# Performance work log

Measured on AMD Instinct MI355X. Metric: run time of the kernel, lower is better.

## Reference

```python
import jax, jax.numpy as jnp
import numpy as np

N_BASIS = 20
R_MAX = 3.5

# e3nn normalize2mom constant for silu: 1/sqrt(E[silu(z)^2]), z~N(0,1) (analytic quadrature)
_trapz = getattr(np, "trapezoid", np.trapz)
_z = np.linspace(-12.0, 12.0, 100001)
_phi = np.exp(-0.5 * _z**2) / np.sqrt(2.0 * np.pi)
_silu = _z / (1.0 + np.exp(-_z))
SILU_CST = float(1.0 / np.sqrt(_trapz(_silu**2 * _phi, _z)))  # ~1.679


def norm_silu(x):
    return SILU_CST * jax.nn.silu(x)


def spherical_harmonics_lmax3(pos):
    # component-normalized real spherical harmonics up to l=3, e3nn axis convention (y up)
    u = pos / jnp.linalg.norm(pos, axis=-1, keepdims=True)
    x, y, z = u[..., 0], u[..., 1], u[..., 2]
    x2, y2, z2 = x * x, y * y, z * z
    s3, s5, s15 = jnp.sqrt(3.0), jnp.sqrt(5.0), jnp.sqrt(15.0)
    s7, s105 = jnp.sqrt(7.0), jnp.sqrt(105.0)
    s35_8, s21_8 = jnp.sqrt(35.0 / 8.0), jnp.sqrt(21.0 / 8.0)
    sh = [
        jnp.ones_like(x),                                                   # l=0
        s3 * x, s3 * y, s3 * z,                                             # l=1
        s15 * x * z, s15 * x * y, s5 * (y2 - 0.5 * (x2 + z2)),
        s15 * y * z, 0.5 * s15 * (z2 - x2),                                 # l=2
        s35_8 * x * (3.0 * z2 - x2), s105 * x * y * z,
        s21_8 * x * (5.0 * y2 - 1.0), 0.5 * s7 * y * (5.0 * y2 - 3.0),
        s21_8 * z * (5.0 * y2 - 1.0), 0.5 * s105 * y * (z2 - x2),
        s35_8 * z * (z2 - 3.0 * x2),                                        # l=3
    ]
    return jnp.stack(sh, axis=-1)  # [E, 16]


def soft_one_hot_gaussian(d):
    # e3nn soft_one_hot_linspace(start=0, end=3.5, number=20, basis='gaussian', cutoff=True)
    values = jnp.linspace(0.0, R_MAX, N_BASIS + 2)[1:-1]
    step = R_MAX / (N_BASIS + 1)
    diff = (d[:, None] - values[None, :]) / step
    return jnp.exp(-diff * diff) / 1.12


def setup_inputs() -> dict:
    E, N = 2_000_000, 125_000
    key = jax.random.key(0)
    k = jax.random.split(key, 6)
    return {
        "pos": jax.random.normal(k[0], (E, 3), jnp.float32),
        "x_right": jax.random.normal(k[1], (E, 1), jnp.float32),
        "x_left": jax.random.normal(k[2], (N, 1), jnp.float32),
        "W1": jax.random.normal(k[3], (20, 30), jnp.float32),
        "W2": jax.random.normal(k[4], (30, 5), jnp.float32),
        "origin_index": jax.random.randint(k[5], (E,), 0, N),
    }


def reference(pos, x_right, x_left, W1, W2, origin_index):
    sh = spherical_harmonics_lmax3(pos)                 # [E, 16], component norm
    d = jnp.linalg.norm(pos, axis=-1)                   # [E]
    emb = soft_one_hot_gaussian(d)                      # [E, 20]
    # e3nn FullyConnectedNet([20, 30, 5], silu): x @ W / sqrt(fan_in), normalized act on hidden
    h = norm_silu(emb @ (W1 / jnp.sqrt(jnp.asarray(W1.shape[0], jnp.float32))))
    tp_weights = h @ (W2 / jnp.sqrt(jnp.asarray(W2.shape[0], jnp.float32)))  # [E, 5]
    # tp1: FullyConnectedTensorProduct('1x0e', sh, '5x0e'): only CG path is 0e(x)0e->0e
    # (single path -> path-normalization factor 1; Y_0 = 1 under component normalization)
    h_right = tp_weights * x_right * sh[:, :1]          # [E, 5]
    # tp2: FullTensorProduct('1x0e', '5x0e') -> '5x0e': plain scalar product per channel
    product = x_left[origin_index] * h_right            # [E, 5]
    return jnp.sum(product)
```

## Files before the change

kernel.cpp:

```cpp
#include <hip/hip_runtime.h>


#define TN    2048
#define DMAXF 5.0f
#define TPB   256
#define EPT   8
#define TILE  (TPB * EPT)

__device__ __constant__ float kSiluCst = 1.6765581f;

__global__ __launch_bounds__(256) void build_lut_kernel(
    const float* __restrict__ W1, const float* __restrict__ W2,
    float* __restrict__ table, float* __restrict__ out)
{
    if (blockIdx.x == 0 && threadIdx.x == 0) out[0] = 0.0f;

    int t = blockIdx.x * 256 + threadIdx.x;
    int entry = t >> 5;
    int k = t & 31;
    int kk = (k < 30) ? k : 29;

    float d  = (float)entry * (DMAXF / (float)TN);
    float t6 = 6.0f * d;
    const float w1scale = 1.0f / (1.12f * sqrtf(20.0f));

    float a = 0.0f;
    #pragma unroll
    for (int j = 0; j < 20; ++j) {
        float df = t6 - (float)(j + 1);
        float e  = __expf(-df * df);
        a = fmaf(e * w1scale, W1[j * 30 + kk], a);
    }
    float s = a / (1.0f + __expf(-a));

    float w2s = 0.0f;
    #pragma unroll
    for (int c = 0; c < 5; ++c) w2s += W2[kk * 5 + c];

    float contrib = (k < 30) ? s * w2s * (kSiluCst / sqrtf(30.0f)) : 0.0f;

    #pragma unroll
    for (int m = 16; m > 0; m >>= 1) contrib += __shfl_xor(contrib, m, 32);

    if (k == 0 && entry < TN) table[entry] = contrib;
}

__global__ __launch_bounds__(TPB) void edge_sum_kernel(
    const float* __restrict__ pos, const float* __restrict__ xr,
    const float* __restrict__ xl, const int* __restrict__ oi,
    const float* __restrict__ table, float* __restrict__ out, int E)
{
    __shared__ float lut[TN];
    __shared__ double swv[TPB / 64];

    const int tid = threadIdx.x;

    {
        const float4* t4 = (const float4*)table;
        float4* l4 = (float4*)lut;
        l4[tid]       = t4[tid];
        l4[tid + TPB] = t4[tid + TPB];
    }
    __syncthreads();

    const float scale = (float)TN / DMAXF;
    const float umax  = (float)(TN - 1) - 1e-3f;

    const long tile0 = (long)blockIdx.x * TILE;
    const int  rem   = (int)min((long)TILE, (long)E - tile0);
    const int  e0    = tid * EPT;
    double acc = 0.0;

    if (e0 + EPT <= rem) {
        const long g0 = tile0 + e0;
        const float4* p4 = (const float4*)(pos + g0 * 3);
        float4 P0 = p4[0], P1 = p4[1], P2 = p4[2], P3 = p4[3], P4 = p4[4], P5 = p4[5];
        const float4* x4 = (const float4*)(xr + g0);
        float4 X0 = x4[0], X1 = x4[1];
        const int4* o4 = (const int4*)(oi + g0);
        int4 O0 = o4[0], O1 = o4[1];

        float xlv[EPT];
        xlv[0] = xl[O0.x]; xlv[1] = xl[O0.y]; xlv[2] = xl[O0.z]; xlv[3] = xl[O0.w];
        xlv[4] = xl[O1.x]; xlv[5] = xl[O1.y]; xlv[6] = xl[O1.z]; xlv[7] = xl[O1.w];

        float px[EPT] = {P0.x, P0.w, P1.z, P2.y, P3.x, P3.w, P4.z, P5.y};
        float py[EPT] = {P0.y, P1.x, P1.w, P2.z, P3.y, P4.x, P4.w, P5.z};
        float pz[EPT] = {P0.z, P1.y, P2.x, P2.w, P3.z, P4.y, P5.x, P5.w};
        float xrv[EPT] = {X0.x, X0.y, X0.z, X0.w, X1.x, X1.y, X1.z, X1.w};

        float fsum = 0.0f;
        #pragma unroll
        for (int j = 0; j < EPT; ++j) {
            float d  = sqrtf(fmaf(px[j], px[j], fmaf(py[j], py[j], pz[j] * pz[j])));
            float u  = fminf(d * scale, umax);
            int   i0 = (int)u;
            float fr = u - (float)i0;
            float f  = fmaf(fr, lut[i0 + 1] - lut[i0], lut[i0]);
            fsum = fmaf(f * xrv[j], xlv[j], fsum);
        }
        acc = (double)fsum;
    } else if (e0 < rem) {
        float fsum = 0.0f;
        for (int j = 0; j < EPT && e0 + j < rem; ++j) {
            long  ge = tile0 + e0 + j;
            float x = pos[3 * ge], y = pos[3 * ge + 1], z = pos[3 * ge + 2];
            float d  = sqrtf(fmaf(x, x, fmaf(y, y, z * z)));
            float u  = fminf(d * scale, umax);
            int   i0 = (int)u;
            float fr = u - (float)i0;
            float f  = fmaf(fr, lut[i0 + 1] - lut[i0], lut[i0]);
            fsum = fmaf(f * xr[ge], xl[oi[ge]], fsum);
        }
        acc = (double)fsum;
    }

    #pragma unroll
    for (int off = 32; off > 0; off >>= 1) acc += __shfl_down(acc, off);
    int lane = tid & 63, wv = tid >> 6;
    if (lane == 0) swv[wv] = acc;
    __syncthreads();
    if (tid == 0) {
        double bsum = (swv[0] + swv[1]) + (swv[2] + swv[3]);
        atomicAdd(out, (float)bsum);
    }
}

extern "C" void kernel_launch(void* const* d_in, const int* in_sizes, int n_in,
                              void* d_out, int out_size, void* d_ws, size_t ws_size,
                              hipStream_t stream) {
    const float* pos = (const float*)d_in[0];
    const float* xr  = (const float*)d_in[1];
    const float* xl  = (const float*)d_in[2];
    const float* W1  = (const float*)d_in[3];
    const float* W2  = (const float*)d_in[4];
    const int*   oi  = (const int*)d_in[5];
    float* out = (float*)d_out;

    int E = in_sizes[1];
    int nblk = (E + TILE - 1) / TILE;

    float* table = (float*)d_ws;

    hipLaunchKernelGGL(build_lut_kernel, dim3((TN * 32) / 256), dim3(256), 0, stream,
                       W1, W2, table, out);
    hipLaunchKernelGGL(edge_sum_kernel, dim3(nblk), dim3(TPB), 0, stream,
                       pos, xr, xl, oi, table, out, E);
}
```

Before: 28.03 us.

## Split edge reduction into a per-edge value kernel and a gather-reduce kernel

Splits the fused edge kernel in two. The first kernel computes the LUT-interpolated radial factor times x_right and writes it to a workspace buffer. The second kernel gathers x_left by origin_index, multiplies, and does the reduction. The likely intent is to separate the gather latency from the LUT and sqrt work so each kernel has simpler register and memory behaviour. The cost is an extra 8 MB write and read of the intermediate per call, plus one more kernel launch.

Measured after the change: 36.50 us. +30.2%, slower.

```diff
diff --git a/kernel.cpp b/kernel.cpp
--- a/kernel.cpp
+++ b/kernel.cpp
@@ -45,14 +45,11 @@
     if (k == 0 && entry < TN) table[entry] = contrib;
 }
 
-__global__ __launch_bounds__(TPB) void edge_sum_kernel(
+__global__ __launch_bounds__(TPB) void val_kernel(
     const float* __restrict__ pos, const float* __restrict__ xr,
-    const float* __restrict__ xl, const int* __restrict__ oi,
-    const float* __restrict__ table, float* __restrict__ out, int E)
+    const float* __restrict__ table, float* __restrict__ val, int E)
 {
     __shared__ float lut[TN];
-    __shared__ double swv[TPB / 64];
-
     const int tid = threadIdx.x;
 
     {
@@ -69,27 +66,20 @@
     const long tile0 = (long)blockIdx.x * TILE;
     const int  rem   = (int)min((long)TILE, (long)E - tile0);
     const int  e0    = tid * EPT;
-    double acc = 0.0;
 
     if (e0 + EPT <= rem) {
         const long g0 = tile0 + e0;
         const float4* p4 = (const float4*)(pos + g0 * 3);
         float4 P0 = p4[0], P1 = p4[1], P2 = p4[2], P3 = p4[3], P4 = p4[4], P5 = p4[5];
-        const float4* x4 = (const float4*)(xr + g0);
-        float4 X0 = x4[0], X1 = x4[1];
-        const int4* o4 = (const int4*)(oi + g0);
-        int4 O0 = o4[0], O1 = o4[1];
-
-        float xlv[EPT];
-        xlv[0] = xl[O0.x]; xlv[1] = xl[O0.y]; xlv[2] = xl[O0.z]; xlv[3] = xl[O0.w];
-        xlv[4] = xl[O1.x]; xlv[5] = xl[O1.y]; xlv[6] = xl[O1.z]; xlv[7] = xl[O1.w];
+        float4 X0 = ((const float4*)(xr + g0))[0];
+        float4 X1 = ((const float4*)(xr + g0))[1];
 
         float px[EPT] = {P0.x, P0.w, P1.z, P2.y, P3.x, P3.w, P4.z, P5.y};
         float py[EPT] = {P0.y, P1.x, P1.w, P2.z, P3.y, P4.x, P4.w, P5.z};
         float pz[EPT] = {P0.z, P1.y, P2.x, P2.w, P3.z, P4.y, P5.x, P5.w};
         float xrv[EPT] = {X0.x, X0.y, X0.z, X0.w, X1.x, X1.y, X1.z, X1.w};
 
-        float fsum = 0.0f;
+        float v[EPT];
         #pragma unroll
         for (int j = 0; j < EPT; ++j) {
             float d  = sqrtf(fmaf(px[j], px[j], fmaf(py[j], py[j], pz[j] * pz[j])));
@@ -97,11 +87,12 @@
             int   i0 = (int)u;
             float fr = u - (float)i0;
             float f  = fmaf(fr, lut[i0 + 1] - lut[i0], lut[i0]);
-            fsum = fmaf(f * xrv[j], xlv[j], fsum);
+            v[j] = f * xrv[j];
         }
-        acc = (double)fsum;
+        float4* o4 = (float4*)(val + g0);
+        o4[0] = make_float4(v[0], v[1], v[2], v[3]);
+        o4[1] = make_float4(v[4], v[5], v[6], v[7]);
     } else if (e0 < rem) {
-        float fsum = 0.0f;
         for (int j = 0; j < EPT && e0 + j < rem; ++j) {
             long  ge = tile0 + e0 + j;
             float x = pos[3 * ge], y = pos[3 * ge + 1], z = pos[3 * ge + 2];
@@ -110,7 +101,44 @@
             int   i0 = (int)u;
             float fr = u - (float)i0;
             float f  = fmaf(fr, lut[i0 + 1] - lut[i0], lut[i0]);
-            fsum = fmaf(f * xr[ge], xl[oi[ge]], fsum);
+            val[ge] = f * xr[ge];
+        }
+    }
+}
+
+__global__ __launch_bounds__(TPB) void gather_kernel(
+    const float* __restrict__ val, const int* __restrict__ oi,
+    const float* __restrict__ xl, float* __restrict__ out, int E)
+{
+    __shared__ double swv[TPB / 64];
+
+    const int  tid   = threadIdx.x;
+    const long tile0 = (long)blockIdx.x * TILE;
+    const int  rem   = (int)min((long)TILE, (long)E - tile0);
+    const int  e0    = tid * EPT;
+    double acc = 0.0;
+
+    if (e0 + EPT <= rem) {
+        const long g0 = tile0 + e0;
+        const int4*   o4 = (const int4*)(oi + g0);
+        const float4* v4 = (const float4*)(val + g0);
+        int4   O0 = o4[0], O1 = o4[1];
+        float4 V0 = v4[0], V1 = v4[1];
+
+        float xlv[EPT];
+        xlv[0] = xl[O0.x]; xlv[1] = xl[O0.y]; xlv[2] = xl[O0.z]; xlv[3] = xl[O0.w];
+        xlv[4] = xl[O1.x]; xlv[5] = xl[O1.y]; xlv[6] = xl[O1.z]; xlv[7] = xl[O1.w];
+
+        float vv[EPT] = {V0.x, V0.y, V0.z, V0.w, V1.x, V1.y, V1.z, V1.w};
+        float fsum = 0.0f;
+        #pragma unroll
+        for (int j = 0; j < EPT; ++j) fsum = fmaf(vv[j], xlv[j], fsum);
+        acc = (double)fsum;
+    } else if (e0 < rem) {
+        float fsum = 0.0f;
+        for (int j = 0; j < EPT && e0 + j < rem; ++j) {
+            long ge = tile0 + e0 + j;
+            fsum = fmaf(val[ge], xl[oi[ge]], fsum);
         }
         acc = (double)fsum;
     }
@@ -141,9 +169,12 @@
     int nblk = (E + TILE - 1) / TILE;
 
     float* table = (float*)d_ws;
+    float* val   = (float*)((char*)d_ws + (size_t)TN * sizeof(float));
 
     hipLaunchKernelGGL(build_lut_kernel, dim3((TN * 32) / 256), dim3(256), 0, stream,
                        W1, W2, table, out);
-    hipLaunchKernelGGL(edge_sum_kernel, dim3(nblk), dim3(TPB), 0, stream,
-                       pos, xr, xl, oi, table, out, E);
+    hipLaunchKernelGGL(val_kernel, dim3(nblk), dim3(TPB), 0, stream,
+                       pos, xr, table, val, E);
+    hipLaunchKernelGGL(gather_kernel, dim3(nblk), dim3(TPB), 0, stream,
+                       val, oi, xl, out, E);
 }
```
